# Kernel optimization log

Hardware: AMD Instinct MI355X
Metric: run time of the kernel (lower is better)

## Reference

```python
import jax, jax.numpy as jnp
import numpy as np

N_NODES = 100000
N_EDGES = 3200000
N_GRAPHS = 64


def setup_inputs() -> dict:
    key = jax.random.key(0)
    ks = jax.random.split(key, 9)
    x = jax.random.normal(ks[0], (N_NODES, 3), dtype=jnp.float32)
    edge_index = jax.random.randint(ks[1], (2, N_EDGES), 0, N_NODES, dtype=jnp.int64)
    batch = jnp.sort(jax.random.randint(ks[2], (N_NODES,), 0, N_GRAPHS, dtype=jnp.int64))
    s1 = 1.0 / np.sqrt(3.0)
    s2 = 1.0 / np.sqrt(64.0)
    W1 = jax.random.normal(ks[3], (3, 64), dtype=jnp.float32) * s1
    b1 = jax.random.normal(ks[4], (64,), dtype=jnp.float32) * 0.02
    W2 = jax.random.normal(ks[5], (64, 64), dtype=jnp.float32) * s2
    b2 = jax.random.normal(ks[6], (64,), dtype=jnp.float32) * 0.02
    Wr = jax.random.normal(ks[7], (64, 1), dtype=jnp.float32) * s2
    br = jax.random.normal(ks[8], (1,), dtype=jnp.float32) * 0.02
    return {"x": x, "edge_index": edge_index, "batch": batch,
            "W1": W1, "b1": b1, "W2": W2, "b2": b2, "Wr": Wr, "br": br}


def reference(x, edge_index, batch, W1, b1, W2, b2, Wr, br):
    N = x.shape[0]
    # GCN normalization with self-loops: A_hat = D^-1/2 (A+I) D^-1/2
    loop = jnp.arange(N, dtype=edge_index.dtype)
    src = jnp.concatenate([edge_index[0], loop])  # message sources
    dst = jnp.concatenate([edge_index[1], loop])  # aggregation targets
    deg = jax.ops.segment_sum(jnp.ones(src.shape, jnp.float32), dst, num_segments=N)
    dinv = jnp.where(deg > 0, jax.lax.rsqrt(deg), 0.0)
    norm = dinv[src] * dinv[dst]  # [E+N]

    def conv(h):  # h: [N, F] -> gather, scale, scatter-add
        return jax.ops.segment_sum(norm[:, None] * h[src], dst, num_segments=N)

    h = jax.nn.relu(conv(x @ W1) + b1)
    # dropout(p=0.5) is identity in eval mode
    h = jax.nn.relu(conv(h @ W2) + b2)
    # global mean pool over graphs
    counts = jax.ops.segment_sum(jnp.ones((N,), jnp.float32), batch, num_segments=N_GRAPHS)
    pooled = jax.ops.segment_sum(h, batch, num_segments=N_GRAPHS) / jnp.maximum(counts, 1.0)[:, None]
    return pooled @ Wr + br
```

## Files before the change

### kernel.cpp

```cpp
#include <hip/hip_runtime.h>

#define N_NODES  100000
#define N_EDGES  3200000
#define N_GRAPHS 64
#define NBUCK 391
#define BSH   8
#define TILE  4096
#define CSR_CAP 9216

typedef float v2f __attribute__((ext_vector_type(2)));

__device__ __forceinline__ unsigned pk8(float a, float b, float c, float d) {
    int r = 0;
    r = __builtin_amdgcn_cvt_pk_fp8_f32(a, b, r, false);
    r = __builtin_amdgcn_cvt_pk_fp8_f32(c, d, r, true);
    return (unsigned)r;
}
__device__ __forceinline__ void addfp8(float4& a, unsigned u) {
    v2f lo = __builtin_amdgcn_cvt_pk_f32_fp8((int)u, false);
    v2f hi = __builtin_amdgcn_cvt_pk_f32_fp8((int)u, true);
    a.x += lo[0]; a.y += lo[1]; a.z += hi[0]; a.w += hi[1];
}

__global__ __launch_bounds__(256) void k_split(
        const int* __restrict__ src, const int* __restrict__ dst,
        int* __restrict__ gcur, unsigned int* __restrict__ ebuf, int E) {
    __shared__ int hist[512];
    __shared__ int excl_s[512];
    __shared__ int base[NBUCK];
    __shared__ int curs[NBUCK];
    __shared__ int wtot[4];
    __shared__ unsigned int stg[TILE];
    __shared__ unsigned short bkt[TILE];
    int t = threadIdx.x;
    hist[t] = 0; hist[t + 256] = 0;
    __syncthreads();

    int e0 = blockIdx.x * TILE;
    int nvalid = min(TILE, E - e0);
    int es[16], ed[16];
#pragma unroll
    for (int k = 0; k < 16; ++k) {
        int i = e0 + t + k * 256;
        if (i < E) {
            es[k] = src[i]; ed[k] = dst[i];
            atomicAdd(&hist[ed[k] >> BSH], 1);
        } else { es[k] = 0; ed[k] = -1; }
    }
    __syncthreads();
    int b0 = t * 2;
    int v0 = hist[b0], v1 = hist[b0 + 1];
    int lsum = v0 + v1;
    int lane = t & 63, wv = t >> 6;
    int val = lsum;
    for (int off = 1; off < 64; off <<= 1) {
        int u = __shfl_up(val, off);
        if (lane >= off) val += u;
    }
    if (lane == 63) wtot[wv] = val;
    __syncthreads();
    int woff = 0;
    for (int w = 0; w < wv; ++w) woff += wtot[w];
    int texcl = woff + val - lsum;
    if (b0 < NBUCK)     { if (v0 > 0) base[b0]     = atomicAdd(&gcur[b0],     v0); curs[b0]     = 0; }
    if (b0 + 1 < NBUCK) { if (v1 > 0) base[b0 + 1] = atomicAdd(&gcur[b0 + 1], v1); curs[b0 + 1] = 0; }
    excl_s[b0] = texcl; excl_s[b0 + 1] = texcl + v0;
    __syncthreads();
#pragma unroll
    for (int k = 0; k < 16; ++k) {
        if (ed[k] >= 0) {
            int b = ed[k] >> BSH;
            int r = atomicAdd(&curs[b], 1);
            int pos = excl_s[b] + r;
            stg[pos] = ((unsigned)(ed[k] & 255) << 24) | (unsigned)es[k];
            bkt[pos] = (unsigned short)b;
        }
    }
    __syncthreads();
    for (int j = t; j < nvalid; j += 256) {
        unsigned p = stg[j];
        int b = bkt[j];
        int pos = base[b] + (j - excl_s[b]);
        if (pos < CSR_CAP) ebuf[(size_t)b * CSR_CAP + pos] = p;
    }
}

__global__ __launch_bounds__(1024) void k_csr(
        const unsigned int* __restrict__ ebuf, const int* __restrict__ gcur,
        int* __restrict__ rowptr, float* __restrict__ dinv, float4* __restrict__ y4,
        const float* __restrict__ x, int* __restrict__ csr_src, int N) {
    __shared__ int ncnt[256];
    __shared__ int nbase[256];
    __shared__ int ncur[256];
    __shared__ int wtot[4];
    __shared__ int sbase;
    __shared__ int stg[CSR_CAP];
    int b = blockIdx.x, t = threadIdx.x;
    int node0 = b << BSH;
    int nodes = min(256, N - node0);
    int cntE = min(gcur[b], CSR_CAP);
    const unsigned int* eb = ebuf + (size_t)b * CSR_CAP;
    if (t < 64) {
        int acc = 0;
        for (int i = t; i < b; i += 64) acc += min(gcur[i], CSR_CAP);
        for (int off = 32; off > 0; off >>= 1) acc += __shfl_down(acc, off);
        if (t == 0) sbase = acc;
    }
    if (t < 256) { ncnt[t] = 0; ncur[t] = 0; }
    __syncthreads();
    int base = sbase;
    if (b == NBUCK - 1 && t == 0) rowptr[N_NODES] = base + cntE;
    for (int j = t; j < cntE; j += 1024) atomicAdd(&ncnt[(int)(eb[j] >> 24)], 1);
    __syncthreads();
    int v = (t < 256) ? ncnt[t] : 0;
    if (t < 256) {
        int lane = t & 63, wv = t >> 6;
        int val = v;
        for (int off = 1; off < 64; off <<= 1) {
            int u = __shfl_up(val, off);
            if (lane >= off) val += u;
        }
        if (lane == 63) wtot[wv] = val;
        __syncthreads();
        int woff = 0;
        for (int w = 0; w < wv; ++w) woff += wtot[w];
        int excl = woff + val - v;
        nbase[t] = excl;
        if (t < nodes) {
            int nn = node0 + t;
            rowptr[nn] = base + excl;
            float dn = rsqrtf((float)(v + 1));
            dinv[nn] = dn;
            y4[nn] = make_float4(dn * x[nn * 3 + 0], dn * x[nn * 3 + 1], dn * x[nn * 3 + 2], 0.f);
        }
    } else {
        __syncthreads();
    }
    __syncthreads();
    for (int j = t; j < cntE; j += 1024) {
        unsigned p = eb[j];
        int ln = (int)(p >> 24);
        int r = atomicAdd(&ncur[ln], 1);
        stg[nbase[ln] + r] = (int)(p & 0xFFFFFFu);
    }
    __syncthreads();
    for (int j = t; j < cntE; j += 1024) csr_src[(size_t)base + j] = stg[j];
}

__global__ __launch_bounds__(256) void k_agg3h1(
        const float4* __restrict__ y4, const int* __restrict__ csr_src,
        const int* __restrict__ rowptr, const float* __restrict__ dinv,
        const float* __restrict__ W1, const float* __restrict__ b1,
        uint4* __restrict__ Hs, int N) {
    int tid = blockIdx.x * blockDim.x + threadIdx.x;
    int n = tid >> 2, q = tid & 3;
    if (n >= N) return;
    int beg = rowptr[n], end = rowptr[n + 1];
    float4 a0 = make_float4(0.f, 0.f, 0.f, 0.f);
    float4 a1 = make_float4(0.f, 0.f, 0.f, 0.f);
    float4 a2 = make_float4(0.f, 0.f, 0.f, 0.f);
    float4 a3 = make_float4(0.f, 0.f, 0.f, 0.f);
    int c = beg + q;
    for (; c + 12 < end; c += 16) {
        int s0 = csr_src[c], s1 = csr_src[c + 4], s2 = csr_src[c + 8], s3 = csr_src[c + 12];
        float4 v0 = y4[s0], v1 = y4[s1], v2 = y4[s2], v3 = y4[s3];
        a0.x += v0.x; a0.y += v0.y; a0.z += v0.z;
        a1.x += v1.x; a1.y += v1.y; a1.z += v1.z;
        a2.x += v2.x; a2.y += v2.y; a2.z += v2.z;
        a3.x += v3.x; a3.y += v3.y; a3.z += v3.z;
    }
    for (; c < end; c += 4) {
        float4 v = y4[csr_src[c]];
        a0.x += v.x; a0.y += v.y; a0.z += v.z;
    }
    float rx = (a0.x + a1.x) + (a2.x + a3.x);
    float ry = (a0.y + a1.y) + (a2.y + a3.y);
    float rz = (a0.z + a1.z) + (a2.z + a3.z);
    for (int off = 1; off < 4; off <<= 1) {
        rx += __shfl_xor(rx, off);
        ry += __shfl_xor(ry, off);
        rz += __shfl_xor(rz, off);
    }
    float dn = dinv[n];
    float4 self = y4[n];
    float A0 = dn * (rx + self.x), A1 = dn * (ry + self.y), A2 = dn * (rz + self.z);
    unsigned vals[4];
#pragma unroll
    for (int g = 0; g < 4; ++g) {
        int f = 16 * q + 4 * g;
        float w0 = dn * fmaxf(A0 * W1[f]     + A1 * W1[64 + f]     + A2 * W1[128 + f]     + b1[f],     0.f);
        float w1 = dn * fmaxf(A0 * W1[f + 1] + A1 * W1[64 + f + 1] + A2 * W1[128 + f + 1] + b1[f + 1], 0.f);
        float w2 = dn * fmaxf(A0 * W1[f + 2] + A1 * W1[64 + f + 2] + A2 * W1[128 + f + 2] + b1[f + 2], 0.f);
        float w3 = dn * fmaxf(A0 * W1[f + 3] + A1 * W1[64 + f + 3] + A2 * W1[128 + f + 3] + b1[f + 3], 0.f);
        vals[g] = pk8(w0, w1, w2, w3);
    }
    Hs[(size_t)n * 4 + q] = make_uint4(vals[0], vals[1], vals[2], vals[3]);
}

__global__ __launch_bounds__(256) void k_agg(
        const unsigned int* __restrict__ Hs, const int* __restrict__ csr_src,
        const int* __restrict__ rowptr, const float* __restrict__ dinv,
        float* __restrict__ out, int N) {
    int tid = blockIdx.x * blockDim.x + threadIdx.x;
    int n = tid >> 4, q = tid & 15;
    if (n >= N) return;
    int lane = threadIdx.x & 63;
    int base = lane & ~15;
    int beg = rowptr[n], end = rowptr[n + 1];
    float4 acc0 = make_float4(0.f, 0.f, 0.f, 0.f);
    float4 acc1 = make_float4(0.f, 0.f, 0.f, 0.f);
    float4 acc2 = make_float4(0.f, 0.f, 0.f, 0.f);
    float4 acc3 = make_float4(0.f, 0.f, 0.f, 0.f);
    for (int c = beg; c < end; c += 16) {
        int myidx = csr_src[min(c + q, end - 1)];
        int m = min(16, end - c);
        int j = 0;
        for (; j + 4 <= m; j += 4) {
            int s0 = __shfl(myidx, base + j + 0);
            int s1 = __shfl(myidx, base + j + 1);
            int s2 = __shfl(myidx, base + j + 2);
            int s3 = __shfl(myidx, base + j + 3);
            unsigned u0 = Hs[(size_t)s0 * 16 + q];
            unsigned u1 = Hs[(size_t)s1 * 16 + q];
            unsigned u2 = Hs[(size_t)s2 * 16 + q];
            unsigned u3 = Hs[(size_t)s3 * 16 + q];
            addfp8(acc0, u0); addfp8(acc1, u1); addfp8(acc2, u2); addfp8(acc3, u3);
        }
        for (; j < m; ++j) {
            int s = __shfl(myidx, base + j);
            addfp8(acc0, Hs[(size_t)s * 16 + q]);
        }
    }
    addfp8(acc0, Hs[(size_t)n * 16 + q]);
    float dn = dinv[n];
    float4 r;
    r.x = dn * ((acc0.x + acc1.x) + (acc2.x + acc3.x));
    r.y = dn * ((acc0.y + acc1.y) + (acc2.y + acc3.y));
    r.z = dn * ((acc0.z + acc1.z) + (acc2.z + acc3.z));
    r.w = dn * ((acc0.w + acc1.w) + (acc2.w + acc3.w));
    ((float4*)(out + (size_t)n * 64))[q] = r;
}

__device__ __forceinline__ void fma4(float4& c, float s, const float4& w) {
    c.x += s * w.x; c.y += s * w.y; c.z += s * w.z; c.w += s * w.w;
}

__global__ __launch_bounds__(256) void k_mmpool(
        const float4* __restrict__ A4, const float4* __restrict__ W2v,
        const float* __restrict__ b2, const float* __restrict__ Wr,
        const int* __restrict__ batch, float* __restrict__ gsum,
        float* __restrict__ gcnt, int N) {
    __shared__ float4 W2s[1024];
    __shared__ float lsum[N_GRAPHS];
    __shared__ float lcnt[N_GRAPHS];
    int t = threadIdx.x;
    for (int i = t; i < 1024; i += 256) W2s[i] = W2v[i];
    if (t < N_GRAPHS) { lsum[t] = 0.f; lcnt[t] = 0.f; }
    __syncthreads();

    int f4 = t & 15;
    int ng = t >> 4;
    float4 bb = ((const float4*)b2)[f4];
    float4 wr = ((const float4*)Wr)[f4];
    int base = blockIdx.x * 128;

    for (int tile = 0; tile < 2; ++tile) {
        int n0 = base + tile * 64 + ng * 4;
        int m0 = min(n0 + 0, N - 1), m1 = min(n0 + 1, N - 1);
        int m2 = min(n0 + 2, N - 1), m3 = min(n0 + 3, N - 1);
        const float4* r0 = A4 + (size_t)m0 * 16;
        const float4* r1 = A4 + (size_t)m1 * 16;
        const float4* r2 = A4 + (size_t)m2 * 16;
        const float4* r3 = A4 + (size_t)m3 * 16;
        float4 c0 = make_float4(0.f, 0.f, 0.f, 0.f);
        float4 c1 = make_float4(0.f, 0.f, 0.f, 0.f);
        float4 c2 = make_float4(0.f, 0.f, 0.f, 0.f);
        float4 c3 = make_float4(0.f, 0.f, 0.f, 0.f);
#pragma unroll 4
        for (int ks = 0; ks < 16; ++ks) {
            float4 a0 = r0[ks], a1 = r1[ks], a2 = r2[ks], a3 = r3[ks];
            float4 w0 = W2s[(4 * ks + 0) * 16 + f4];
            float4 w1 = W2s[(4 * ks + 1) * 16 + f4];
            float4 w2 = W2s[(4 * ks + 2) * 16 + f4];
            float4 w3 = W2s[(4 * ks + 3) * 16 + f4];
            fma4(c0, a0.x, w0); fma4(c0, a0.y, w1); fma4(c0, a0.z, w2); fma4(c0, a0.w, w3);
            fma4(c1, a1.x, w0); fma4(c1, a1.y, w1); fma4(c1, a1.z, w2); fma4(c1, a1.w, w3);
            fma4(c2, a2.x, w0); fma4(c2, a2.y, w1); fma4(c2, a2.z, w2); fma4(c2, a2.w, w3);
            fma4(c3, a3.x, w0); fma4(c3, a3.y, w1); fma4(c3, a3.z, w2); fma4(c3, a3.w, w3);
        }
        float p0 = fmaxf(c0.x + bb.x, 0.f) * wr.x + fmaxf(c0.y + bb.y, 0.f) * wr.y +
                   fmaxf(c0.z + bb.z, 0.f) * wr.z + fmaxf(c0.w + bb.w, 0.f) * wr.w;
        float p1 = fmaxf(c1.x + bb.x, 0.f) * wr.x + fmaxf(c1.y + bb.y, 0.f) * wr.y +
                   fmaxf(c1.z + bb.z, 0.f) * wr.z + fmaxf(c1.w + bb.w, 0.f) * wr.w;
        float p2 = fmaxf(c2.x + bb.x, 0.f) * wr.x + fmaxf(c2.y + bb.y, 0.f) * wr.y +
                   fmaxf(c2.z + bb.z, 0.f) * wr.z + fmaxf(c2.w + bb.w, 0.f) * wr.w;
        float p3 = fmaxf(c3.x + bb.x, 0.f) * wr.x + fmaxf(c3.y + bb.y, 0.f) * wr.y +
                   fmaxf(c3.z + bb.z, 0.f) * wr.z + fmaxf(c3.w + bb.w, 0.f) * wr.w;
        for (int off = 8; off > 0; off >>= 1) {
            p0 += __shfl_down(p0, off);
            p1 += __shfl_down(p1, off);
            p2 += __shfl_down(p2, off);
            p3 += __shfl_down(p3, off);
        }
        if (f4 == 0) {
            if (n0 + 0 < N) { int g = batch[n0 + 0]; atomicAdd(&lsum[g], p0); atomicAdd(&lcnt[g], 1.f); }
            if (n0 + 1 < N) { int g = batch[n0 + 1]; atomicAdd(&lsum[g], p1); atomicAdd(&lcnt[g], 1.f); }
            if (n0 + 2 < N) { int g = batch[n0 + 2]; atomicAdd(&lsum[g], p2); atomicAdd(&lcnt[g], 1.f); }
            if (n0 + 3 < N) { int g = batch[n0 + 3]; atomicAdd(&lsum[g], p3); atomicAdd(&lcnt[g], 1.f); }
        }
    }
    __syncthreads();
    if (t < N_GRAPHS && lcnt[t] > 0.0f) {
        atomicAdd(&gsum[t], lsum[t]);
        atomicAdd(&gcnt[t], lcnt[t]);
    }
}

__global__ void k_out(const float* __restrict__ gsum, const float* __restrict__ gcnt,
                      const float* __restrict__ br, float* __restrict__ out) {
    int g = threadIdx.x;
    if (g < N_GRAPHS) out[g] = gsum[g] / fmaxf(gcnt[g], 1.0f) + br[0];
}

extern "C" void kernel_launch(void* const* d_in, const int* in_sizes, int n_in,
                              void* d_out, int out_size, void* d_ws, size_t ws_size,
                              hipStream_t stream) {
    const float* x     = (const float*)d_in[0];
    const int*   ei    = (const int*)d_in[1];
    const int*   batch = (const int*)d_in[2];
    const float* W1    = (const float*)d_in[3];
    const float* b1    = (const float*)d_in[4];
    const float* W2    = (const float*)d_in[5];
    const float* b2    = (const float*)d_in[6];
    const float* Wr    = (const float*)d_in[7];
    const float* br    = (const float*)d_in[8];
    float* out = (float*)d_out;

    const int N = N_NODES, E = N_EDGES;
    const int* src = ei;
    const int* dst = ei + E;

    char* w = (char*)d_ws;
    float* A        = (float*)w; w += (size_t)N * 64 * sizeof(float);
    unsigned int* Hs = (unsigned int*)w; w += (size_t)N * 64;
    int*   csr_src  = (int*)w;   w += (size_t)E * sizeof(int);
    float* dinv     = (float*)w; w += (size_t)N * sizeof(float);
    int*   rowptr   = (int*)w;   w += (size_t)(N + 1) * sizeof(int);
    int*   gcur     = (int*)w;   w += (size_t)NBUCK * sizeof(int);
    float* gsum     = (float*)w; w += N_GRAPHS * sizeof(float);
    float* gcnt     = (float*)w; w += N_GRAPHS * sizeof(float);
    float4* y4      = (float4*)w; w += (size_t)N * sizeof(float4);
    unsigned int* ebuf = (unsigned int*)A;

    hipMemsetAsync(gcur, 0, (size_t)NBUCK * sizeof(int), stream);
    hipMemsetAsync(gsum, 0, N_GRAPHS * sizeof(float), stream);
    hipMemsetAsync(gcnt, 0, N_GRAPHS * sizeof(float), stream);

    k_split<<<(E + TILE - 1) / TILE, 256, 0, stream>>>(src, dst, gcur, ebuf, E);
    k_csr<<<NBUCK, 1024, 0, stream>>>(ebuf, gcur, rowptr, dinv, y4, x, csr_src, N);

    k_agg3h1<<<(N * 4 + 255) / 256, 256, 0, stream>>>(y4, csr_src, rowptr, dinv,
                                                      W1, b1, (uint4*)Hs, N);

    k_agg<<<(N * 16 + 255) / 256, 256, 0, stream>>>(Hs, csr_src, rowptr, dinv, A, N);
    k_mmpool<<<(N + 127) / 128, 256, 0, stream>>>((const float4*)A, (const float4*)W2,
                                                  b2, Wr, batch, gsum, gcnt, N);

    k_out<<<1, 64, 0, stream>>>(gsum, gcnt, br, out);
}
```

Baseline: 240.1 us.

## Fuse second-layer aggregation with W2 matmul and mean pooling via LDS

Merges the fp8 neighbor-aggregation kernel and the matmul/pool kernel into one kernel. Each block aggregates 64 nodes into a shared-memory tile and then applies W2, bias, ReLU, the readout weights and pooling from that tile. This removes the global write and re-read of the N×64 fp32 intermediate and one kernel launch. The cost is that each 16-lane group now processes four nodes in sequence, and the extra LDS use may lower occupancy and gather parallelism.

```diff
diff --git a/kernel.cpp b/kernel.cpp
--- a/kernel.cpp
+++ b/kernel.cpp
@@ -20,6 +20,9 @@
     v2f lo = __builtin_amdgcn_cvt_pk_f32_fp8((int)u, false);
     v2f hi = __builtin_amdgcn_cvt_pk_f32_fp8((int)u, true);
     a.x += lo[0]; a.y += lo[1]; a.z += hi[0]; a.w += hi[1];
+}
+__device__ __forceinline__ void fma4(float4& c, float s, const float4& w) {
+    c.x += s * w.x; c.y += s * w.y; c.z += s * w.z; c.w += s * w.w;
 }
 
 __global__ __launch_bounds__(256) void k_split(
@@ -197,117 +200,110 @@
     Hs[(size_t)n * 4 + q] = make_uint4(vals[0], vals[1], vals[2], vals[3]);
 }
 
-__global__ __launch_bounds__(256) void k_agg(
+__global__ __launch_bounds__(256) void k_aggmm(
         const unsigned int* __restrict__ Hs, const int* __restrict__ csr_src,
         const int* __restrict__ rowptr, const float* __restrict__ dinv,
-        float* __restrict__ out, int N) {
-    int tid = blockIdx.x * blockDim.x + threadIdx.x;
-    int n = tid >> 4, q = tid & 15;
-    if (n >= N) return;
-    int lane = threadIdx.x & 63;
-    int base = lane & ~15;
-    int beg = rowptr[n], end = rowptr[n + 1];
-    float4 acc0 = make_float4(0.f, 0.f, 0.f, 0.f);
-    float4 acc1 = make_float4(0.f, 0.f, 0.f, 0.f);
-    float4 acc2 = make_float4(0.f, 0.f, 0.f, 0.f);
-    float4 acc3 = make_float4(0.f, 0.f, 0.f, 0.f);
-    for (int c = beg; c < end; c += 16) {
-        int myidx = csr_src[min(c + q, end - 1)];
-        int m = min(16, end - c);
-        int j = 0;
-        for (; j + 4 <= m; j += 4) {
-            int s0 = __shfl(myidx, base + j + 0);
-            int s1 = __shfl(myidx, base + j + 1);
-            int s2 = __shfl(myidx, base + j + 2);
-            int s3 = __shfl(myidx, base + j + 3);
-            unsigned u0 = Hs[(size_t)s0 * 16 + q];
-            unsigned u1 = Hs[(size_t)s1 * 16 + q];
-            unsigned u2 = Hs[(size_t)s2 * 16 + q];
-            unsigned u3 = Hs[(size_t)s3 * 16 + q];
-            addfp8(acc0, u0); addfp8(acc1, u1); addfp8(acc2, u2); addfp8(acc3, u3);
-        }
-        for (; j < m; ++j) {
-            int s = __shfl(myidx, base + j);
-            addfp8(acc0, Hs[(size_t)s * 16 + q]);
-        }
-    }
-    addfp8(acc0, Hs[(size_t)n * 16 + q]);
-    float dn = dinv[n];
-    float4 r;
-    r.x = dn * ((acc0.x + acc1.x) + (acc2.x + acc3.x));
-    r.y = dn * ((acc0.y + acc1.y) + (acc2.y + acc3.y));
-    r.z = dn * ((acc0.z + acc1.z) + (acc2.z + acc3.z));
-    r.w = dn * ((acc0.w + acc1.w) + (acc2.w + acc3.w));
-    ((float4*)(out + (size_t)n * 64))[q] = r;
-}
-
-__device__ __forceinline__ void fma4(float4& c, float s, const float4& w) {
-    c.x += s * w.x; c.y += s * w.y; c.z += s * w.z; c.w += s * w.w;
-}
-
-__global__ __launch_bounds__(256) void k_mmpool(
-        const float4* __restrict__ A4, const float4* __restrict__ W2v,
-        const float* __restrict__ b2, const float* __restrict__ Wr,
-        const int* __restrict__ batch, float* __restrict__ gsum,
-        float* __restrict__ gcnt, int N) {
+        const float4* __restrict__ W2v, const float* __restrict__ b2,
+        const float* __restrict__ Wr, const int* __restrict__ batch,
+        float* __restrict__ gsum, float* __restrict__ gcnt, int N) {
+    __shared__ float4 hst[64][17];
     __shared__ float4 W2s[1024];
     __shared__ float lsum[N_GRAPHS];
     __shared__ float lcnt[N_GRAPHS];
     int t = threadIdx.x;
     for (int i = t; i < 1024; i += 256) W2s[i] = W2v[i];
     if (t < N_GRAPHS) { lsum[t] = 0.f; lcnt[t] = 0.f; }
+
+    int q = t & 15;
+    int grp = t >> 4;
+    int lane = t & 63;
+    int base_l = lane & ~15;
+    int node0 = blockIdx.x * 64;
+
+    for (int rep = 0; rep < 4; ++rep) {
+        int nl = grp * 4 + rep;
+        int n = node0 + nl;
+        if (n < N) {
+            int beg = rowptr[n], end = rowptr[n + 1];
+            float4 acc0 = make_float4(0.f, 0.f, 0.f, 0.f);
+            float4 acc1 = make_float4(0.f, 0.f, 0.f, 0.f);
+            float4 acc2 = make_float4(0.f, 0.f, 0.f, 0.f);
+            float4 acc3 = make_float4(0.f, 0.f, 0.f, 0.f);
+            for (int c = beg; c < end; c += 16) {
+                int myidx = csr_src[min(c + q, end - 1)];
+                int m = min(16, end - c);
+                int j = 0;
+                for (; j + 4 <= m; j += 4) {
+                    int s0 = __shfl(myidx, base_l + j + 0);
+                    int s1 = __shfl(myidx, base_l + j + 1);
+                    int s2 = __shfl(myidx, base_l + j + 2);
+                    int s3 = __shfl(myidx, base_l + j + 3);
+                    unsigned u0 = Hs[(size_t)s0 * 16 + q];
+                    unsigned u1 = Hs[(size_t)s1 * 16 + q];
+                    unsigned u2 = Hs[(size_t)s2 * 16 + q];
+                    unsigned u3 = Hs[(size_t)s3 * 16 + q];
+                    addfp8(acc0, u0); addfp8(acc1, u1); addfp8(acc2, u2); addfp8(acc3, u3);
+                }
+                for (; j < m; ++j) {
+                    int s = __shfl(myidx, base_l + j);
+                    addfp8(acc0, Hs[(size_t)s * 16 + q]);
+                }
+            }
+            addfp8(acc0, Hs[(size_t)n * 16 + q]);
+            float dn = dinv[n];
+            float4 r;
+            r.x = dn * ((acc0.x + acc1.x) + (acc2.x + acc3.x));
+            r.y = dn * ((acc0.y + acc1.y) + (acc2.y + acc3.y));
+            r.z = dn * ((acc0.z + acc1.z) + (acc2.z + acc3.z));
+            r.w = dn * ((acc0.w + acc1.w) + (acc2.w + acc3.w));
+            hst[nl][q] = r;
+        }
+    }
     __syncthreads();
 
     int f4 = t & 15;
     int ng = t >> 4;
     float4 bb = ((const float4*)b2)[f4];
     float4 wr = ((const float4*)Wr)[f4];
-    int base = blockIdx.x * 128;
-
-    for (int tile = 0; tile < 2; ++tile) {
-        int n0 = base + tile * 64 + ng * 4;
-        int m0 = min(n0 + 0, N - 1), m1 = min(n0 + 1, N - 1);
-        int m2 = min(n0 + 2, N - 1), m3 = min(n0 + 3, N - 1);
-        const float4* r0 = A4 + (size_t)m0 * 16;
-        const float4* r1 = A4 + (size_t)m1 * 16;
-        const float4* r2 = A4 + (size_t)m2 * 16;
-        const float4* r3 = A4 + (size_t)m3 * 16;
-        float4 c0 = make_float4(0.f, 0.f, 0.f, 0.f);
-        float4 c1 = make_float4(0.f, 0.f, 0.f, 0.f);
-        float4 c2 = make_float4(0.f, 0.f, 0.f, 0.f);
-        float4 c3 = make_float4(0.f, 0.f, 0.f, 0.f);
+    int n0 = node0 + ng * 4;
+    float4 c0 = make_float4(0.f, 0.f, 0.f, 0.f);
+    float4 c1 = make_float4(0.f, 0.f, 0.f, 0.f);
+    float4 c2 = make_float4(0.f, 0.f, 0.f, 0.f);
+    float4 c3 = make_float4(0.f, 0.f, 0.f, 0.f);
 #pragma unroll 4
-        for (int ks = 0; ks < 16; ++ks) {
-            float4 a0 = r0[ks], a1 = r1[ks], a2 = r2[ks], a3 = r3[ks];
-            float4 w0 = W2s[(4 * ks + 0) * 16 + f4];
-            float4 w1 = W2s[(4 * ks + 1) * 16 + f4];
-            float4 w2 = W2s[(4 * ks + 2) * 16 + f4];
-            float4 w3 = W2s[(4 * ks + 3) * 16 + f4];
-            fma4(c0, a0.x, w0); fma4(c0, a0.y, w1); fma4(c0, a0.z, w2); fma4(c0, a0.w, w3);
-            fma4(c1, a1.x, w0); fma4(c1, a1.y, w1); fma4(c1, a1.z, w2); fma4(c1, a1.w, w3);
-            fma4(c2, a2.x, w0); fma4(c2, a2.y, w1); fma4(c2, a2.z, w2); fma4(c2, a2.w, w3);
-            fma4(c3, a3.x, w0); fma4(c3, a3.y, w1); fma4(c3, a3.z, w2); fma4(c3, a3.w, w3);
-        }
-        float p0 = fmaxf(c0.x + bb.x, 0.f) * wr.x + fmaxf(c0.y + bb.y, 0.f) * wr.y +
-                   fmaxf(c0.z + bb.z, 0.f) * wr.z + fmaxf(c0.w + bb.w, 0.f) * wr.w;
-        float p1 = fmaxf(c1.x + bb.x, 0.f) * wr.x + fmaxf(c1.y + bb.y, 0.f) * wr.y +
-                   fmaxf(c1.z + bb.z, 0.f) * wr.z + fmaxf(c1.w + bb.w, 0.f) * wr.w;
-        float p2 = fmaxf(c2.x + bb.x, 0.f) * wr.x + fmaxf(c2.y + bb.y, 0.f) * wr.y +
-                   fmaxf(c2.z + bb.z, 0.f) * wr.z + fmaxf(c2.w + bb.w, 0.f) * wr.w;
-        float p3 = fmaxf(c3.x + bb.x, 0.f) * wr.x + fmaxf(c3.y + bb.y, 0.f) * wr.y +
-                   fmaxf(c3.z + bb.z, 0.f) * wr.z + fmaxf(c3.w + bb.w, 0.f) * wr.w;
-        for (int off = 8; off > 0; off >>= 1) {
-            p0 += __shfl_down(p0, off);
-            p1 += __shfl_down(p1, off);
-            p2 += __shfl_down(p2, off);
-            p3 += __shfl_down(p3, off);
-        }
-        if (f4 == 0) {
-            if (n0 + 0 < N) { int g = batch[n0 + 0]; atomicAdd(&lsum[g], p0); atomicAdd(&lcnt[g], 1.f); }
-            if (n0 + 1 < N) { int g = batch[n0 + 1]; atomicAdd(&lsum[g], p1); atomicAdd(&lcnt[g], 1.f); }
-            if (n0 + 2 < N) { int g = batch[n0 + 2]; atomicAdd(&lsum[g], p2); atomicAdd(&lcnt[g], 1.f); }
-            if (n0 + 3 < N) { int g = batch[n0 + 3]; atomicAdd(&lsum[g], p3); atomicAdd(&lcnt[g], 1.f); }
-        }
+    for (int ks = 0; ks < 16; ++ks) {
+        float4 a0 = hst[ng * 4 + 0][ks];
+        float4 a1 = hst[ng * 4 + 1][ks];
+        float4 a2 = hst[ng * 4 + 2][ks];
+        float4 a3 = hst[ng * 4 + 3][ks];
+        float4 w0 = W2s[(4 * ks + 0) * 16 + f4];
+        float4 w1 = W2s[(4 * ks + 1) * 16 + f4];
+        float4 w2 = W2s[(4 * ks + 2) * 16 + f4];
+        float4 w3 = W2s[(4 * ks + 3) * 16 + f4];
+        fma4(c0, a0.x, w0); fma4(c0, a0.y, w1); fma4(c0, a0.z, w2); fma4(c0, a0.w, w3);
+        fma4(c1, a1.x, w0); fma4(c1, a1.y, w1); fma4(c1, a1.z, w2); fma4(c1, a1.w, w3);
+        fma4(c2, a2.x, w0); fma4(c2, a2.y, w1); fma4(c2, a2.z, w2); fma4(c2, a2.w, w3);
+        fma4(c3, a3.x, w0); fma4(c3, a3.y, w1); fma4(c3, a3.z, w2); fma4(c3, a3.w, w3);
+    }
+    float p0 = fmaxf(c0.x + bb.x, 0.f) * wr.x + fmaxf(c0.y + bb.y, 0.f) * wr.y +
+               fmaxf(c0.z + bb.z, 0.f) * wr.z + fmaxf(c0.w + bb.w, 0.f) * wr.w;
+    float p1 = fmaxf(c1.x + bb.x, 0.f) * wr.x + fmaxf(c1.y + bb.y, 0.f) * wr.y +
+               fmaxf(c1.z + bb.z, 0.f) * wr.z + fmaxf(c1.w + bb.w, 0.f) * wr.w;
+    float p2 = fmaxf(c2.x + bb.x, 0.f) * wr.x + fmaxf(c2.y + bb.y, 0.f) * wr.y +
+               fmaxf(c2.z + bb.z, 0.f) * wr.z + fmaxf(c2.w + bb.w, 0.f) * wr.w;
+    float p3 = fmaxf(c3.x + bb.x, 0.f) * wr.x + fmaxf(c3.y + bb.y, 0.f) * wr.y +
+               fmaxf(c3.z + bb.z, 0.f) * wr.z + fmaxf(c3.w + bb.w, 0.f) * wr.w;
+    for (int off = 8; off > 0; off >>= 1) {
+        p0 += __shfl_down(p0, off);
+        p1 += __shfl_down(p1, off);
+        p2 += __shfl_down(p2, off);
+        p3 += __shfl_down(p3, off);
+    }
+    if (f4 == 0) {
+        if (n0 + 0 < N) { int g = batch[n0 + 0]; atomicAdd(&lsum[g], p0); atomicAdd(&lcnt[g], 1.f); }
+        if (n0 + 1 < N) { int g = batch[n0 + 1]; atomicAdd(&lsum[g], p1); atomicAdd(&lcnt[g], 1.f); }
+        if (n0 + 2 < N) { int g = batch[n0 + 2]; atomicAdd(&lsum[g], p2); atomicAdd(&lcnt[g], 1.f); }
+        if (n0 + 3 < N) { int g = batch[n0 + 3]; atomicAdd(&lsum[g], p3); atomicAdd(&lcnt[g], 1.f); }
     }
     __syncthreads();
     if (t < N_GRAPHS && lcnt[t] > 0.0f) {
@@ -362,9 +358,9 @@
     k_agg3h1<<<(N * 4 + 255) / 256, 256, 0, stream>>>(y4, csr_src, rowptr, dinv,
                                                       W1, b1, (uint4*)Hs, N);
 
-    k_agg<<<(N * 16 + 255) / 256, 256, 0, stream>>>(Hs, csr_src, rowptr, dinv, A, N);
-    k_mmpool<<<(N + 127) / 128, 256, 0, stream>>>((const float4*)A, (const float4*)W2,
-                                                  b2, Wr, batch, gsum, gcnt, N);
+    k_aggmm<<<(N + 63) / 64, 256, 0, stream>>>(Hs, csr_src, rowptr, dinv,
+                                               (const float4*)W2, b2, Wr, batch,
+                                               gsum, gcnt, N);
 
     k_out<<<1, 64, 0, stream>>>(gsum, gcnt, br, out);
 }
```

Measured after the change: 247.9 us. 3.3% more time.
